# Kernel optimization log

Hardware: AMD Instinct MI355X
Metric: run time of the kernel (lower is better)

The kernel has to match this reference:

```python
import jax, jax.numpy as jnp
import numpy as np

D_MODEL = 1024
NHEAD = 16
HEAD_DIM = D_MODEL // NHEAD
WINDOW = 33  # mask keeps |i-j| > WINDOW//2 (True = attend, matching torch SDPA bool-mask semantics)


def setup_inputs() -> dict:
    key = jax.random.key(0)
    ks = jax.random.split(key, 9)
    s = 1.0 / np.sqrt(D_MODEL)
    x = jax.random.normal(ks[0], (2, 2048, D_MODEL), dtype=jnp.float32)
    Wq = jax.random.uniform(ks[1], (D_MODEL, D_MODEL), jnp.float32, -s, s)
    bq = jax.random.uniform(ks[2], (D_MODEL,), jnp.float32, -s, s)
    Wk = jax.random.uniform(ks[3], (D_MODEL, D_MODEL), jnp.float32, -s, s)
    bk = jax.random.uniform(ks[4], (D_MODEL,), jnp.float32, -s, s)
    Wv = jax.random.uniform(ks[5], (D_MODEL, D_MODEL), jnp.float32, -s, s)
    bv = jax.random.uniform(ks[6], (D_MODEL,), jnp.float32, -s, s)
    Wo = jax.random.uniform(ks[7], (D_MODEL, D_MODEL), jnp.float32, -s, s)
    bo = jax.random.uniform(ks[8], (D_MODEL,), jnp.float32, -s, s)
    return {"x": x, "Wq": Wq, "bq": bq, "Wk": Wk, "bk": bk,
            "Wv": Wv, "bv": bv, "Wo": Wo, "bo": bo}


def reference(x, Wq, bq, Wk, bk, Wv, bv, Wo, bo):
    B, T, C = x.shape
    H, D = NHEAD, HEAD_DIM
    # projections (torch Linear: y = x @ W.T + b)
    q = (x @ Wq.T + bq).reshape(B, T, H, D).transpose(0, 2, 1, 3)  # [B,H,T,D]
    k = (x @ Wk.T + bk).reshape(B, T, H, D).transpose(0, 2, 1, 3)
    v = (x @ Wv.T + bv).reshape(B, T, H, D).transpose(0, 2, 1, 3)
    idx = jnp.arange(T)
    rel = jnp.abs(idx[:, None] - idx[None, :])
    keep = rel > (WINDOW // 2)  # True = participate (torch SDPA bool-mask semantics)
    scale = 1.0 / jnp.sqrt(jnp.asarray(D, dtype=x.dtype))
    scores = jnp.einsum('bhqd,bhkd->bhqk', q, k) * scale
    scores = jnp.where(keep, scores, jnp.asarray(-jnp.inf, dtype=scores.dtype))
    attn = jax.nn.softmax(scores, axis=-1)
    out = jnp.einsum('bhqk,bhkd->bhqd', attn, v)  # [B,H,T,D]
    out = out.transpose(0, 2, 1, 3).reshape(B, T, C)
    return out @ Wo.T + bo
```

## Files before the change

### kernel.cpp

```cpp
#include <hip/hip_runtime.h>
#include <stdint.h>


typedef unsigned short u16;
typedef short bf16x8 __attribute__((ext_vector_type(8)));
typedef float f32x4 __attribute__((ext_vector_type(4)));

#define MFMA16 __builtin_amdgcn_mfma_f32_16x16x32_bf16

__device__ __forceinline__ u16 f2bf(float f) {
  union { float f; uint32_t u; } v; v.f = f;
  return (u16)((v.u + 0x7fffu + ((v.u >> 16) & 1u)) >> 16);
}

__device__ __forceinline__ uint32_t cvt_pk_bf16(float lo, float hi) {
  uint32_t d;
  asm("v_cvt_pk_bf16_f32 %0, %1, %2" : "=v"(d) : "v"(lo), "v"(hi));
  return d;
}

__device__ __forceinline__ float hexp2(float x) {
  float r;
  asm("v_exp_f32 %0, %1" : "=v"(r) : "v"(x));
  return r;
}

__global__ void f2b5_kernel(const float* __restrict__ x,
                            const float* __restrict__ a, const float* __restrict__ b,
                            const float* __restrict__ c, const float* __restrict__ d,
                            u16* __restrict__ ox, u16* __restrict__ oa, u16* __restrict__ ob,
                            u16* __restrict__ oc, u16* __restrict__ od) {
  int bid = blockIdx.x;
  const float* src; u16* dst; int base;
  if (bid < 4096)      { src = x; dst = ox; base = 0; }
  else if (bid < 5120) { src = a; dst = oa; base = 4096; }
  else if (bid < 6144) { src = b; dst = ob; base = 5120; }
  else if (bid < 7168) { src = c; dst = oc; base = 6144; }
  else                 { src = d; dst = od; base = 7168; }
  int i = (bid - base) * 256 + threadIdx.x;
  float4 v = reinterpret_cast<const float4*>(src)[i];
  ushort4 o;
  o.x = f2bf(v.x); o.y = f2bf(v.y); o.z = f2bf(v.z); o.w = f2bf(v.w);
  reinterpret_cast<ushort4*>(dst)[i] = o;
}

#define GEMM_LOAD(REGA, REGB, A_, B_, KOFF)                                                        \
  do {                                                                                             \
    REGA##0 = *reinterpret_cast<const uint4*>(A_ + (size_t)(gm_base +  0) * 1024 + (KOFF) + sslot * 8); \
    REGA##1 = *reinterpret_cast<const uint4*>(A_ + (size_t)(gm_base + 32) * 1024 + (KOFF) + sslot * 8); \
    REGA##2 = *reinterpret_cast<const uint4*>(A_ + (size_t)(gm_base + 64) * 1024 + (KOFF) + sslot * 8); \
    REGA##3 = *reinterpret_cast<const uint4*>(A_ + (size_t)(gm_base + 96) * 1024 + (KOFF) + sslot * 8); \
    REGB##0 = *reinterpret_cast<const uint4*>(B_ + (size_t)(gn_base +  0) * 1024 + (KOFF) + sslot * 8); \
    REGB##1 = *reinterpret_cast<const uint4*>(B_ + (size_t)(gn_base + 32) * 1024 + (KOFF) + sslot * 8); \
    REGB##2 = *reinterpret_cast<const uint4*>(B_ + (size_t)(gn_base + 64) * 1024 + (KOFF) + sslot * 8); \
    REGB##3 = *reinterpret_cast<const uint4*>(B_ + (size_t)(gn_base + 96) * 1024 + (KOFF) + sslot * 8); \
  } while (0)

#define GEMM_PUBLISH()                                                                             \
  do {                                                                                             \
    *reinterpret_cast<uint4*>((char*)As + (srow +  0) * 144 + sslot * 16) = ar0;                   \
    *reinterpret_cast<uint4*>((char*)As + (srow + 32) * 144 + sslot * 16) = ar1;                   \
    *reinterpret_cast<uint4*>((char*)As + (srow + 64) * 144 + sslot * 16) = ar2;                   \
    *reinterpret_cast<uint4*>((char*)As + (srow + 96) * 144 + sslot * 16) = ar3;                   \
    *reinterpret_cast<uint4*>((char*)Bs + (srow +  0) * 144 + sslot * 16) = br0;                   \
    *reinterpret_cast<uint4*>((char*)Bs + (srow + 32) * 144 + sslot * 16) = br1;                   \
    *reinterpret_cast<uint4*>((char*)Bs + (srow + 64) * 144 + sslot * 16) = br2;                   \
    *reinterpret_cast<uint4*>((char*)Bs + (srow + 96) * 144 + sslot * 16) = br3;                   \
  } while (0)

#define GEMM_CORE(A_, B_, bm0_, bn0_)                                                              \
  constexpr int KP = 72;                                                                           \
  __shared__ __align__(16) u16 As[128 * KP];                                                       \
  __shared__ __align__(16) u16 Bs[128 * KP];                                                       \
  const int t = threadIdx.x;                                                                       \
  const int lane = t & 63;                                                                         \
  const int wv = t >> 6;                                                                           \
  const int wm = (wv >> 1) * 64;                                                                   \
  const int wn = (wv & 1) * 64;                                                                    \
  const int lg = lane >> 4;                                                                        \
  const int lr = lane & 15;                                                                        \
  const int srow = t >> 3;                                                                         \
  const int sslot = t & 7;                                                                         \
  const int gm_base = bm0_ + srow;                                                                 \
  const int gn_base = bn0_ + srow;                                                                 \
  uint4 ar0, ar1, ar2, ar3, br0, br1, br2, br3;                                                    \
  f32x4 acc[4][4];                                                                                 \
  for (int i = 0; i < 4; ++i)                                                                      \
    for (int j = 0; j < 4; ++j) acc[i][j] = (f32x4)0.0f;                                           \
  GEMM_LOAD(ar, br, A_, B_, 0);                                                                    \
  for (int k0 = 0; k0 < 1024; k0 += 64) {                                                          \
    GEMM_PUBLISH();                                                                                \
    __syncthreads();                                                                               \
    if (k0 + 64 < 1024) GEMM_LOAD(ar, br, A_, B_, k0 + 64);                                        \
    for (int kk = 0; kk < 2; ++kk) {                                                               \
      bf16x8 af[4], bfr[4];                                                                        \
      for (int i = 0; i < 4; ++i)                                                                  \
        af[i] = *reinterpret_cast<const bf16x8*>(&As[(wm + i * 16 + lr) * KP + kk * 32 + lg * 8]); \
      for (int j = 0; j < 4; ++j)                                                                  \
        bfr[j] = *reinterpret_cast<const bf16x8*>(&Bs[(wn + j * 16 + lr) * KP + kk * 32 + lg * 8]);\
      for (int i = 0; i < 4; ++i)                                                                  \
        for (int j = 0; j < 4; ++j)                                                                \
          acc[i][j] = MFMA16(af[i], bfr[j], acc[i][j], 0, 0, 0);                                   \
    }                                                                                              \
    __syncthreads();                                                                               \
  }

__global__ __launch_bounds__(256) void gemm_qkv(
    const u16* __restrict__ A,
    const u16* __restrict__ Wqb, const u16* __restrict__ Wkb, const u16* __restrict__ Wvb,
    const float* __restrict__ bqp, const float* __restrict__ bkp, const float* __restrict__ bvp,
    u16* __restrict__ qo, u16* __restrict__ ko, u16* __restrict__ vo)
{
  const int bid = blockIdx.x + gridDim.x * blockIdx.y;
  const int sid = (bid & 7) * 96 + (bid >> 3);
  const int bm0 = (sid / 24) * 128;
  const int jy = sid % 24;
  const int sel = jy >> 3;
  const int bn0 = (jy & 7) * 128;

  const u16* Bw = (sel == 0) ? Wqb : (sel == 1) ? Wkb : Wvb;
  const float* bias = (sel == 0) ? bqp : (sel == 1) ? bkp : bvp;
  const float scale = (sel == 0) ? 0.125f * 1.44269504f : 1.0f;

  GEMM_CORE(A, Bw, bm0, bn0)

  for (int j = 0; j < 4; ++j) {
    int gn = bn0 + wn + j * 16 + lr;
    float bv = bias[gn];
    for (int i = 0; i < 4; ++i) {
      for (int r = 0; r < 4; ++r) {
        int gm = bm0 + wm + i * 16 + lg * 4 + r;
        float val = (acc[i][j][r] + bv) * scale;
        int b = gm >> 11, tt = gm & 2047;
        int h = gn >> 6,  d = gn & 63;
        u16 o = f2bf(val);
        if (sel == 0)
          qo[((size_t)(b * 16 + h) * 2048 + tt) * 64 + d] = o;
        else if (sel == 1)
          ko[((size_t)(b * 16 + h) * 2048 + tt) * 64 + d] = o;
        else
          vo[((size_t)(b * 16 + h) * 64 + d) * 2048 + tt] = o;
      }
    }
  }
}

__global__ __launch_bounds__(256) void gemm_out(
    const u16* __restrict__ A, const u16* __restrict__ Bw,
    const float* __restrict__ bias, float* __restrict__ outp)
{
  const int bm0 = blockIdx.x * 128;
  const int bn0 = blockIdx.y * 128;

  GEMM_CORE(A, Bw, bm0, bn0)

  for (int j = 0; j < 4; ++j) {
    int gn = bn0 + wn + j * 16 + lr;
    float bv = bias[gn];
    for (int i = 0; i < 4; ++i)
      for (int r = 0; r < 4; ++r) {
        int gm = bm0 + wm + i * 16 + lg * 4 + r;
        outp[(size_t)gm * 1024 + gn] = acc[i][j][r] + bv;
      }
  }
}

__global__ __launch_bounds__(256, 2) void attn_kernel(
    const u16* __restrict__ qb, const u16* __restrict__ kb,
    const u16* __restrict__ vtb, u16* __restrict__ ab)
{
  constexpr int KP = 72;
  __shared__ __align__(16) u16 Kb[2][64 * KP];
  __shared__ __align__(16) u16 Vb[2][64 * KP];
  __shared__ __align__(16) u16 Pl[4][32 * 64];

  const int bid = blockIdx.x + gridDim.x * blockIdx.y;
  const int sid = (bid & 7) * 64 + (bid >> 3);
  const int bx = sid & 15;
  const int bh = sid >> 4;

  const int t = threadIdx.x;
  const int lane = t & 63;
  const int wv = t >> 6;
  const int lg = lane >> 4, lr = lane & 15;
  const int q0 = bx * 128 + wv * 32;

  const u16* Qp = qb + (size_t)bh * 2048 * 64;
  const u16* Kp = kb + (size_t)bh * 2048 * 64;
  const u16* Vt = vtb + (size_t)bh * 64 * 2048;
  char* Pw = (char*)&Pl[wv][0];
  const int swz = (lr & 7) << 4;

  const int sl = lane & 7;
  const int r0 = wv * 16 + (lane >> 3);
  const int sdst0 = r0 * (KP * 2) + sl * 16;

  uint4 krA, krB, vrA, vrB;

#define ISSUE_LOADS(J0N)                                                                 \
  do {                                                                                   \
    krA = *reinterpret_cast<const uint4*>(Kp + (size_t)((J0N) + r0) * 64 + sl * 8);      \
    krB = *reinterpret_cast<const uint4*>(Kp + (size_t)((J0N) + r0 + 8) * 64 + sl * 8);  \
    vrA = *reinterpret_cast<const uint4*>(Vt + (size_t)r0 * 2048 + (J0N) + sl * 8);      \
    vrB = *reinterpret_cast<const uint4*>(Vt + (size_t)(r0 + 8) * 2048 + (J0N) + sl * 8);\
  } while (0)

#define WRITE_LDS(BUF)                                                                   \
  do {                                                                                   \
    *reinterpret_cast<uint4*>((char*)&Kb[BUF][0] + sdst0)                = krA;          \
    *reinterpret_cast<uint4*>((char*)&Kb[BUF][0] + sdst0 + 8 * KP * 2)   = krB;          \
    *reinterpret_cast<uint4*>((char*)&Vb[BUF][0] + sdst0)                = vrA;          \
    *reinterpret_cast<uint4*>((char*)&Vb[BUF][0] + sdst0 + 8 * KP * 2)   = vrB;          \
  } while (0)

  bf16x8 qf[2][2];
  for (int qi = 0; qi < 2; ++qi)
    for (int h = 0; h < 2; ++h)
      qf[qi][h] = *reinterpret_cast<const bf16x8*>(&Qp[(size_t)(q0 + qi * 16 + lr) * 64 + h * 32 + lg * 8]);

  f32x4 o[2][4];
  for (int qi = 0; qi < 2; ++qi)
    for (int d = 0; d < 4; ++d) o[qi][d] = (f32x4)0.0f;
  float m[2] = {-1e30f, -1e30f};
  float lsum[2] = {0.0f, 0.0f};

  ISSUE_LOADS(0);
  WRITE_LDS(0);
  __syncthreads();
  int cur = 0;

  for (int tt = 0; tt < 32; ++tt) {
    if (tt < 31) ISSUE_LOADS((tt + 1) * 64);
    const int j0 = tt * 64;

    f32x4 s[2][4];
    __builtin_amdgcn_s_setprio(1);
    for (int kc = 0; kc < 4; ++kc) {
      bf16x8 kf0 = *reinterpret_cast<const bf16x8*>(&Kb[cur][(kc * 16 + lr) * KP + lg * 8]);
      bf16x8 kf1 = *reinterpret_cast<const bf16x8*>(&Kb[cur][(kc * 16 + lr) * KP + 32 + lg * 8]);
      for (int qi = 0; qi < 2; ++qi) {
        f32x4 z = (f32x4)0.0f;
        z = MFMA16(kf0, qf[qi][0], z, 0, 0, 0);
        z = MFMA16(kf1, qf[qi][1], z, 0, 0, 0);
        s[qi][kc] = z;
      }
    }
    __builtin_amdgcn_s_setprio(0);
    if (j0 + 63 >= q0 - 16 && j0 <= q0 + 47) {
      for (int qi = 0; qi < 2; ++qi)
        for (int kc = 0; kc < 4; ++kc)
          for (int r = 0; r < 4; ++r) {
            int i = q0 + qi * 16 + lr;
            int j = j0 + kc * 16 + lg * 4 + r;
            int dd = i - j; if (dd < 0) dd = -dd;
            if (dd <= 16) s[qi][kc][r] = -1e38f;
          }
    }
    float pm[2];
    for (int qi = 0; qi < 2; ++qi) {
      f32x4 t4 = __builtin_elementwise_max(__builtin_elementwise_max(s[qi][0], s[qi][1]),
                                           __builtin_elementwise_max(s[qi][2], s[qi][3]));
      float x = fmaxf(fmaxf(t4[0], t4[1]), fmaxf(t4[2], t4[3]));
      x = fmaxf(x, __shfl_xor(x, 16));
      x = fmaxf(x, __shfl_xor(x, 32));
      pm[qi] = x;
    }
    bool need = (pm[0] > m[0] + 11.54f) || (pm[1] > m[1] + 11.54f);
    if (__any((int)need)) {
      for (int qi = 0; qi < 2; ++qi) {
        float mn = fmaxf(m[qi], pm[qi]);
        float a = hexp2(m[qi] - mn);
        m[qi] = mn;
        lsum[qi] *= a;
        for (int d = 0; d < 4; ++d) o[qi][d] *= a;
      }
    }
    for (int qi = 0; qi < 2; ++qi) {
      int rowbase = (qi * 16 + lr) * 128;
      float psum = 0.0f;
      for (int kc = 0; kc < 4; ++kc) {
        float p0 = hexp2(s[qi][kc][0] - m[qi]);
        float p1 = hexp2(s[qi][kc][1] - m[qi]);
        float p2 = hexp2(s[qi][kc][2] - m[qi]);
        float p3 = hexp2(s[qi][kc][3] - m[qi]);
        psum += (p0 + p1) + (p2 + p3);
        uint2 pk;
        pk.x = cvt_pk_bf16(p0, p1);
        pk.y = cvt_pk_bf16(p2, p3);
        *reinterpret_cast<uint2*>(Pw + ((rowbase + kc * 32 + lg * 8) ^ swz)) = pk;
      }
      lsum[qi] += psum;
    }
    asm volatile("s_waitcnt lgkmcnt(0)" ::: "memory");
    __builtin_amdgcn_s_setprio(1);
    for (int kh = 0; kh < 2; ++kh) {
      bf16x8 pa[2];
      for (int qi = 0; qi < 2; ++qi)
        pa[qi] = *reinterpret_cast<const bf16x8*>(
            Pw + (((qi * 16 + lr) * 128 + kh * 64 + lg * 16) ^ swz));
      for (int d = 0; d < 4; ++d) {
        bf16x8 vf = *reinterpret_cast<const bf16x8*>(
            &Vb[cur][(d * 16 + lr) * KP + kh * 32 + lg * 8]);
        for (int qi = 0; qi < 2; ++qi)
          o[qi][d] = MFMA16(vf, pa[qi], o[qi][d], 0, 0, 0);
      }
    }
    __builtin_amdgcn_s_setprio(0);
    if (tt < 31) WRITE_LDS(cur ^ 1);
    __syncthreads();
    cur ^= 1;
  }

  int b = bh >> 4, h = bh & 15;
  for (int qi = 0; qi < 2; ++qi) {
    float ls = lsum[qi];
    ls += __shfl_xor(ls, 16);
    ls += __shfl_xor(ls, 32);
    float inv = 1.0f / ls;
    size_t rowoff = ((size_t)b * 2048 + q0 + qi * 16 + lr) * 1024 + h * 64;
    for (int d = 0; d < 4; ++d) {
      uint2 pk;
      pk.x = cvt_pk_bf16(o[qi][d][0] * inv, o[qi][d][1] * inv);
      pk.y = cvt_pk_bf16(o[qi][d][2] * inv, o[qi][d][3] * inv);
      *reinterpret_cast<uint2*>(&ab[rowoff + d * 16 + lg * 4]) = pk;
    }
  }
#undef ISSUE_LOADS
#undef WRITE_LDS
}

extern "C" void kernel_launch(void* const* d_in, const int* in_sizes, int n_in,
                              void* d_out, int out_size, void* d_ws, size_t ws_size,
                              hipStream_t stream) {
  const float* x  = (const float*)d_in[0];
  const float* Wq = (const float*)d_in[1];
  const float* bq = (const float*)d_in[2];
  const float* Wk = (const float*)d_in[3];
  const float* bk = (const float*)d_in[4];
  const float* Wv = (const float*)d_in[5];
  const float* bv = (const float*)d_in[6];
  const float* Wo = (const float*)d_in[7];
  const float* bo = (const float*)d_in[8];

  u16* ws  = (u16*)d_ws;
  u16* xb  = ws;
  u16* wqb = ws + 4194304;
  u16* wkb = ws + 5242880;
  u16* wvb = ws + 6291456;
  u16* wob = ws + 7340032;
  u16* qbf = ws + 8388608;
  u16* kbf = ws + 12582912;
  u16* vbf = ws + 16777216;
  u16* ab  = xb;

  f2b5_kernel<<<8192, 256, 0, stream>>>(x, Wq, Wk, Wv, Wo, xb, wqb, wkb, wvb, wob);

  gemm_qkv<<<dim3(32, 24), 256, 0, stream>>>(xb, wqb, wkb, wvb, bq, bk, bv, qbf, kbf, vbf);

  attn_kernel<<<dim3(16, 32), 256, 0, stream>>>(qbf, kbf, vbf, ab);

  gemm_out<<<dim3(32, 8), 256, 0, stream>>>(ab, wob, bo, (float*)d_out);
}
```

Baseline: 134.9 us.

## Load K/V fragments directly from global into registers, dropping LDS staging

Replaces the double-buffered LDS staging of K and V tiles (with block-wide syncs) by per-wave direct global loads of MFMA operand fragments into registers. The next tile's loads are issued right after the matching MFMAs, giving a register-level prefetch. This removes the __syncthreads barriers and LDS traffic, but each of the 4 waves now fetches the full K/V tiles itself (4x global/L2 reads), uses more registers, and the launch bounds no longer request 2 blocks per CU.

Result: slower. 192.8 us (+43.0%).

```diff
diff --git a/kernel.cpp b/kernel.cpp
--- a/kernel.cpp
+++ b/kernel.cpp
@@ -165,13 +165,10 @@
   }
 }
 
-__global__ __launch_bounds__(256, 2) void attn_kernel(
+__global__ __launch_bounds__(256) void attn_kernel(
     const u16* __restrict__ qb, const u16* __restrict__ kb,
     const u16* __restrict__ vtb, u16* __restrict__ ab)
 {
-  constexpr int KP = 72;
-  __shared__ __align__(16) u16 Kb[2][64 * KP];
-  __shared__ __align__(16) u16 Vb[2][64 * KP];
   __shared__ __align__(16) u16 Pl[4][32 * 64];
 
   const int bid = blockIdx.x + gridDim.x * blockIdx.y;
@@ -186,31 +183,36 @@
   const int q0 = bx * 128 + wv * 32;
 
   const u16* Qp = qb + (size_t)bh * 2048 * 64;
-  const u16* Kp = kb + (size_t)bh * 2048 * 64;
-  const u16* Vt = vtb + (size_t)bh * 64 * 2048;
+  const u16* Kp = kb + (size_t)bh * 2048 * 64 + (size_t)lr * 64 + lg * 8;
+  const u16* Vt = vtb + (size_t)bh * 64 * 2048 + (size_t)lr * 2048 + lg * 8;
   char* Pw = (char*)&Pl[wv][0];
   const int swz = (lr & 7) << 4;
 
-  const int sl = lane & 7;
-  const int r0 = wv * 16 + (lane >> 3);
-  const int sdst0 = r0 * (KP * 2) + sl * 16;
-
-  uint4 krA, krB, vrA, vrB;
-
-#define ISSUE_LOADS(J0N)                                                                 \
-  do {                                                                                   \
-    krA = *reinterpret_cast<const uint4*>(Kp + (size_t)((J0N) + r0) * 64 + sl * 8);      \
-    krB = *reinterpret_cast<const uint4*>(Kp + (size_t)((J0N) + r0 + 8) * 64 + sl * 8);  \
-    vrA = *reinterpret_cast<const uint4*>(Vt + (size_t)r0 * 2048 + (J0N) + sl * 8);      \
-    vrB = *reinterpret_cast<const uint4*>(Vt + (size_t)(r0 + 8) * 2048 + (J0N) + sl * 8);\
+  bf16x8 kA0, kB0, kA1, kB1, kA2, kB2, kA3, kB3;
+  bf16x8 vA0, vB0, vA1, vB1, vA2, vB2, vA3, vB3;
+
+#define LOAD_K(J0)                                                                        \
+  do {                                                                                    \
+    kA0 = *reinterpret_cast<const bf16x8*>(Kp + (size_t)((J0) +  0) * 64 +  0);           \
+    kB0 = *reinterpret_cast<const bf16x8*>(Kp + (size_t)((J0) +  0) * 64 + 32);           \
+    kA1 = *reinterpret_cast<const bf16x8*>(Kp + (size_t)((J0) + 16) * 64 +  0);           \
+    kB1 = *reinterpret_cast<const bf16x8*>(Kp + (size_t)((J0) + 16) * 64 + 32);           \
+    kA2 = *reinterpret_cast<const bf16x8*>(Kp + (size_t)((J0) + 32) * 64 +  0);           \
+    kB2 = *reinterpret_cast<const bf16x8*>(Kp + (size_t)((J0) + 32) * 64 + 32);           \
+    kA3 = *reinterpret_cast<const bf16x8*>(Kp + (size_t)((J0) + 48) * 64 +  0);           \
+    kB3 = *reinterpret_cast<const bf16x8*>(Kp + (size_t)((J0) + 48) * 64 + 32);           \
   } while (0)
 
-#define WRITE_LDS(BUF)                                                                   \
-  do {                                                                                   \
-    *reinterpret_cast<uint4*>((char*)&Kb[BUF][0] + sdst0)                = krA;          \
-    *reinterpret_cast<uint4*>((char*)&Kb[BUF][0] + sdst0 + 8 * KP * 2)   = krB;          \
-    *reinterpret_cast<uint4*>((char*)&Vb[BUF][0] + sdst0)                = vrA;          \
-    *reinterpret_cast<uint4*>((char*)&Vb[BUF][0] + sdst0 + 8 * KP * 2)   = vrB;          \
+#define LOAD_V(J0)                                                                        \
+  do {                                                                                    \
+    vA0 = *reinterpret_cast<const bf16x8*>(Vt + (size_t)0 * 32768 + (J0) +  0);           \
+    vB0 = *reinterpret_cast<const bf16x8*>(Vt + (size_t)0 * 32768 + (J0) + 32);           \
+    vA1 = *reinterpret_cast<const bf16x8*>(Vt + (size_t)1 * 32768 + (J0) +  0);           \
+    vB1 = *reinterpret_cast<const bf16x8*>(Vt + (size_t)1 * 32768 + (J0) + 32);           \
+    vA2 = *reinterpret_cast<const bf16x8*>(Vt + (size_t)2 * 32768 + (J0) +  0);           \
+    vB2 = *reinterpret_cast<const bf16x8*>(Vt + (size_t)2 * 32768 + (J0) + 32);           \
+    vA3 = *reinterpret_cast<const bf16x8*>(Vt + (size_t)3 * 32768 + (J0) +  0);           \
+    vB3 = *reinterpret_cast<const bf16x8*>(Vt + (size_t)3 * 32768 + (J0) + 32);           \
   } while (0)
 
   bf16x8 qf[2][2];
@@ -224,28 +226,29 @@
   float m[2] = {-1e30f, -1e30f};
   float lsum[2] = {0.0f, 0.0f};
 
-  ISSUE_LOADS(0);
-  WRITE_LDS(0);
-  __syncthreads();
-  int cur = 0;
+  LOAD_K(0);
+  LOAD_V(0);
 
   for (int tt = 0; tt < 32; ++tt) {
-    if (tt < 31) ISSUE_LOADS((tt + 1) * 64);
     const int j0 = tt * 64;
 
     f32x4 s[2][4];
     __builtin_amdgcn_s_setprio(1);
-    for (int kc = 0; kc < 4; ++kc) {
-      bf16x8 kf0 = *reinterpret_cast<const bf16x8*>(&Kb[cur][(kc * 16 + lr) * KP + lg * 8]);
-      bf16x8 kf1 = *reinterpret_cast<const bf16x8*>(&Kb[cur][(kc * 16 + lr) * KP + 32 + lg * 8]);
-      for (int qi = 0; qi < 2; ++qi) {
-        f32x4 z = (f32x4)0.0f;
-        z = MFMA16(kf0, qf[qi][0], z, 0, 0, 0);
-        z = MFMA16(kf1, qf[qi][1], z, 0, 0, 0);
-        s[qi][kc] = z;
-      }
+    {
+      f32x4 z;
+#define QK_KC(KC, KA, KB)                                                                 \
+      z = (f32x4)0.0f; z = MFMA16(KA, qf[0][0], z, 0, 0, 0);                              \
+      z = MFMA16(KB, qf[0][1], z, 0, 0, 0); s[0][KC] = z;                                 \
+      z = (f32x4)0.0f; z = MFMA16(KA, qf[1][0], z, 0, 0, 0);                              \
+      z = MFMA16(KB, qf[1][1], z, 0, 0, 0); s[1][KC] = z;
+      QK_KC(0, kA0, kB0)
+      QK_KC(1, kA1, kB1)
+      QK_KC(2, kA2, kB2)
+      QK_KC(3, kA3, kB3)
+#undef QK_KC
     }
     __builtin_amdgcn_s_setprio(0);
+    if (tt < 31) LOAD_K(j0 + 64);
     if (j0 + 63 >= q0 - 16 && j0 <= q0 + 47) {
       for (int qi = 0; qi < 2; ++qi)
         for (int kc = 0; kc < 4; ++kc)
@@ -293,22 +296,30 @@
     }
     asm volatile("s_waitcnt lgkmcnt(0)" ::: "memory");
     __builtin_amdgcn_s_setprio(1);
-    for (int kh = 0; kh < 2; ++kh) {
-      bf16x8 pa[2];
-      for (int qi = 0; qi < 2; ++qi)
-        pa[qi] = *reinterpret_cast<const bf16x8*>(
-            Pw + (((qi * 16 + lr) * 128 + kh * 64 + lg * 16) ^ swz));
-      for (int d = 0; d < 4; ++d) {
-        bf16x8 vf = *reinterpret_cast<const bf16x8*>(
-            &Vb[cur][(d * 16 + lr) * KP + kh * 32 + lg * 8]);
-        for (int qi = 0; qi < 2; ++qi)
-          o[qi][d] = MFMA16(vf, pa[qi], o[qi][d], 0, 0, 0);
-      }
+    {
+      bf16x8 pa0 = *reinterpret_cast<const bf16x8*>(Pw + (((0 * 16 + lr) * 128 + lg * 16) ^ swz));
+      bf16x8 pa1 = *reinterpret_cast<const bf16x8*>(Pw + (((1 * 16 + lr) * 128 + lg * 16) ^ swz));
+      o[0][0] = MFMA16(vA0, pa0, o[0][0], 0, 0, 0);
+      o[0][1] = MFMA16(vA1, pa0, o[0][1], 0, 0, 0);
+      o[0][2] = MFMA16(vA2, pa0, o[0][2], 0, 0, 0);
+      o[0][3] = MFMA16(vA3, pa0, o[0][3], 0, 0, 0);
+      o[1][0] = MFMA16(vA0, pa1, o[1][0], 0, 0, 0);
+      o[1][1] = MFMA16(vA1, pa1, o[1][1], 0, 0, 0);
+      o[1][2] = MFMA16(vA2, pa1, o[1][2], 0, 0, 0);
+      o[1][3] = MFMA16(vA3, pa1, o[1][3], 0, 0, 0);
+      pa0 = *reinterpret_cast<const bf16x8*>(Pw + (((0 * 16 + lr) * 128 + 64 + lg * 16) ^ swz));
+      pa1 = *reinterpret_cast<const bf16x8*>(Pw + (((1 * 16 + lr) * 128 + 64 + lg * 16) ^ swz));
+      o[0][0] = MFMA16(vB0, pa0, o[0][0], 0, 0, 0);
+      o[0][1] = MFMA16(vB1, pa0, o[0][1], 0, 0, 0);
+      o[0][2] = MFMA16(vB2, pa0, o[0][2], 0, 0, 0);
+      o[0][3] = MFMA16(vB3, pa0, o[0][3], 0, 0, 0);
+      o[1][0] = MFMA16(vB0, pa1, o[1][0], 0, 0, 0);
+      o[1][1] = MFMA16(vB1, pa1, o[1][1], 0, 0, 0);
+      o[1][2] = MFMA16(vB2, pa1, o[1][2], 0, 0, 0);
+      o[1][3] = MFMA16(vB3, pa1, o[1][3], 0, 0, 0);
     }
     __builtin_amdgcn_s_setprio(0);
-    if (tt < 31) WRITE_LDS(cur ^ 1);
-    __syncthreads();
-    cur ^= 1;
+    if (tt < 31) LOAD_V(j0 + 64);
   }
 
   int b = bh >> 4, h = bh & 15;
@@ -325,8 +336,8 @@
       *reinterpret_cast<uint2*>(&ab[rowoff + d * 16 + lg * 4]) = pk;
     }
   }
-#undef ISSUE_LOADS
-#undef WRITE_LDS
+#undef LOAD_K
+#undef LOAD_V
 }
 
 extern "C" void kernel_launch(void* const* d_in, const int* in_sizes, int n_in,
```
